# Kernel tuning notes

Hardware: AMD Instinct MI355X
Metric: run time of the kernel (lower is better)

Reference implementation:

```python
import jax, jax.numpy as jnp
import numpy as np

N, E, G = 100000, 300000, 2048
H, C = 4, 64            # heads, per-head channels; hidden = H*C = 256
NODE_DIM, EDGE_DIM, HID = 256, 64, 256
NEG_SLOPE = 0.2
L = 3


def setup_inputs() -> dict:
    key = jax.random.key(0)
    ks = jax.random.split(key, 24)
    s = 0.05
    x = jax.random.normal(ks[0], (N, NODE_DIM), jnp.float32)
    src = jax.random.randint(ks[1], (E,), 0, N)
    dst = jax.random.randint(ks[2], (E,), 0, N)
    dst = jnp.where(src == dst, (dst + 1) % N, dst)  # no pre-existing self loops
    edge_index = jnp.stack([src, dst]).astype(jnp.int32)
    edge_attr = jax.random.normal(ks[3], (E, EDGE_DIM), jnp.float32)
    batch = jnp.sort(jax.random.randint(ks[4], (N,), 0, G)).astype(jnp.int32)
    # GATv2 layer params stacked over L layers (in_dim == HID for all layers)
    Wl = jax.random.normal(ks[5], (L, NODE_DIM, HID), jnp.float32) * s
    bl = jax.random.normal(ks[6], (L, HID), jnp.float32) * s
    Wr = jax.random.normal(ks[7], (L, NODE_DIM, HID), jnp.float32) * s
    br = jax.random.normal(ks[8], (L, HID), jnp.float32) * s
    We = jax.random.normal(ks[9], (L, EDGE_DIM, HID), jnp.float32) * s
    att = jax.random.normal(ks[10], (L, H, C), jnp.float32) * s
    bias = jax.random.normal(ks[11], (L, HID), jnp.float32) * s
    # predictor MLP
    Wp1 = jax.random.normal(ks[12], (HID, HID // 2), jnp.float32) * s
    bp1 = jax.random.normal(ks[13], (HID // 2,), jnp.float32) * s
    Wp2 = jax.random.normal(ks[14], (HID // 2, 1), jnp.float32) * s
    bp2 = jax.random.normal(ks[15], (1,), jnp.float32) * s
    return {"x": x, "edge_index": edge_index, "edge_attr": edge_attr, "batch": batch,
            "Wl": Wl, "bl": bl, "Wr": Wr, "br": br, "We": We, "att": att, "bias": bias,
            "Wp1": Wp1, "bp1": bp1, "Wp2": Wp2, "bp2": bp2}


def _gatv2_layer(x, src, dst, eattr, Wl, bl, Wr, br, We, att, bias):
    n = x.shape[0]
    xl = (x @ Wl + bl).reshape(n, H, C)  # lin_l (source side)
    xr = (x @ Wr + br).reshape(n, H, C)  # lin_r (target side)
    e = (eattr @ We).reshape(-1, H, C)   # lin_edge (no bias)
    m = jax.nn.leaky_relu(xl[src] + xr[dst] + e, NEG_SLOPE)  # [Etot,H,C]
    logits = jnp.einsum('ehc,hc->eh', m, att)                # [Etot,H]
    # segment softmax over destination nodes
    lmax = jax.ops.segment_max(logits, dst, num_segments=n)
    p = jnp.exp(logits - lmax[dst])
    denom = jax.ops.segment_sum(p, dst, num_segments=n)
    alpha = p / (denom[dst] + 1e-16)
    out = jax.ops.segment_sum(xl[src] * alpha[:, :, None], dst, num_segments=n)
    return out.reshape(n, H * C) + bias


def reference(x, edge_index, edge_attr, batch, Wl, bl, Wr, br, We, att, bias, Wp1, bp1, Wp2, bp2):
    n = x.shape[0]
    src, dst = edge_index[0], edge_index[1]
    # add self loops with edge_attr fill_value='mean' (PyG default)
    loop = jnp.arange(n, dtype=src.dtype)
    src_f = jnp.concatenate([src, loop])
    dst_f = jnp.concatenate([dst, loop])
    eattr_f = jnp.concatenate([edge_attr, jnp.broadcast_to(edge_attr.mean(0), (n, edge_attr.shape[1]))], 0)
    for l in range(L):
        x = jax.nn.relu(_gatv2_layer(x, src_f, dst_f, eattr_f,
                                     Wl[l], bl[l], Wr[l], br[l], We[l], att[l], bias[l]))
    # global mean pool over graphs
    sums = jax.ops.segment_sum(x, batch, num_segments=G)
    cnt = jax.ops.segment_sum(jnp.ones((n,), x.dtype), batch, num_segments=G)
    pooled = sums / jnp.maximum(cnt, 1.0)[:, None]
    h = jax.nn.relu(pooled @ Wp1 + bp1)
    return (h @ Wp2 + bp2).squeeze(-1)  # [G]
```

## Files before the change

### kernel.cpp

```cpp
#include <hip/hip_runtime.h>
#include <hip/hip_bf16.h>

#define N_ 100000
#define E_ 300000
#define ETOT 400000
#define G_ 2048
#define NB_SCAN 98
#define NB_SCAN2 391

typedef __attribute__((ext_vector_type(8))) short bf16x8;
typedef __attribute__((ext_vector_type(4))) float f32x4;

__device__ __forceinline__ short f2bf(float f) {
    __hip_bfloat16 h = __float2bfloat16(f);
    return *reinterpret_cast<short*>(&h);
}
__device__ __forceinline__ float bf2f(short s) {
    __hip_bfloat16 h = *reinterpret_cast<__hip_bfloat16*>(&s);
    return __bfloat162float(h);
}

typedef __attribute__((address_space(1))) void* gas_ptr;
typedef __attribute__((address_space(3))) void* las_ptr;
__device__ __forceinline__ void gload16(const void* g, void* l) {
    __builtin_amdgcn_global_load_lds((gas_ptr)g, (las_ptr)l, 16, 0, 0);
}

__device__ __forceinline__ int xcd_swz(int bid, int nwg) {
    int q = nwg >> 3, rr = nwg & 7;
    int xcd = bid & 7, i = bid >> 3;
    return (xcd < rr) ? xcd * (q + 1) + i : rr * (q + 1) + (xcd - rr) * q + i;
}

__global__ __launch_bounds__(256) void mean_kernel(const float* __restrict__ ea, float* __restrict__ meansum) {
    __shared__ float s[256];
    int tid = threadIdx.x;
    int col = tid & 63, rg = tid >> 6;
    float acc = 0.f;
    for (long long row = (long long)blockIdx.x * 4 + rg; row < E_; row += (long long)gridDim.x * 4)
        acc += ea[row * 64 + col];
    s[tid] = acc;
    __syncthreads();
    if (tid < 64) atomicAdd(meansum + tid, s[tid] + s[tid + 64] + s[tid + 128] + s[tid + 192]);
}

__global__ __launch_bounds__(256) void loope_kernel(const float* __restrict__ meansum,
                                                    const float* __restrict__ We_l,
                                                    float* __restrict__ loope) {
    int c = threadIdx.x;
    float acc = 0.f;
    const float invE = 1.0f / (float)E_;
    for (int k = 0; k < 64; k++) acc += (meansum[k] * invE) * We_l[k * 256 + c];
    loope[c] = acc;
}

__device__ __forceinline__ int swz_col(int row, int k) {
    int c = (k >> 3) & 3;
    int s = (row >> 1) & 3;
    return (k & ~31) | ((c ^ s) << 3) | (k & 7);
}

__global__ __launch_bounds__(256) void prep_wcat_kernel(const float* __restrict__ Wl, const float* __restrict__ Wr,
                                                        short* __restrict__ hi, short* __restrict__ lo) {
    int idx = blockIdx.x * 256 + threadIdx.x;
    if (idx >= 3 * 512 * 256) return;
    int l = idx / (512 * 256);
    int rem = idx % (512 * 256);
    int n = rem >> 8, k = rem & 255;
    float v = (n < 256) ? Wl[((size_t)l * 256 + k) * 256 + n]
                        : Wr[((size_t)l * 256 + k) * 256 + (n - 256)];
    short h = f2bf(v);
    size_t o = (size_t)l * 512 * 256 + (size_t)n * 256 + swz_col(n, k);
    hi[o] = h;
    lo[o] = f2bf(v - bf2f(h));
}

__global__ __launch_bounds__(256) void prep_we_kernel(const float* __restrict__ We,
                                                      short* __restrict__ hi) {
    int idx = blockIdx.x * 256 + threadIdx.x;
    if (idx >= 3 * 256 * 64) return;
    int l = idx / (256 * 64);
    int rem = idx % (256 * 64);
    int n = rem >> 6, k = rem & 63;
    float v = We[((size_t)l * 64 + k) * 256 + n];
    hi[(size_t)l * 256 * 64 + (size_t)n * 64 + swz_col(n, k)] = f2bf(v);
}

__global__ __launch_bounds__(256) void split_x_kernel(const float* __restrict__ in,
                                                      short* __restrict__ hi, short* __restrict__ lo) {
    int idx = blockIdx.x * 256 + threadIdx.x;
    if (idx >= N_ * 32) return;
    int gm = idx >> 5, cw = idx & 31;
    int c = cw & 3, win = cw >> 2;
    int s = (gm >> 1) & 3;
    const float* src = in + (size_t)gm * 256 + (win << 5) + (c << 3);
    float4 f0 = *(const float4*)src;
    float4 f1 = *(const float4*)(src + 4);
    float f[8] = {f0.x, f0.y, f0.z, f0.w, f1.x, f1.y, f1.z, f1.w};
    bf16x8 vh, vl;
#pragma unroll
    for (int j = 0; j < 8; j++) {
        short h = f2bf(f[j]);
        vh[j] = h;
        vl[j] = f2bf(f[j] - bf2f(h));
    }
    size_t o = (size_t)gm * 256 + (win << 5) + ((c ^ s) << 3);
    *(bf16x8*)(hi + o) = vh;
    *(bf16x8*)(lo + o) = vl;
}

__global__ __launch_bounds__(256) void split_e_kernel(const float* __restrict__ in, short* __restrict__ hi,
                                                      const int* __restrict__ pose, const int* __restrict__ rnk) {
    int idx = blockIdx.x * 256 + threadIdx.x;
    if (idx >= E_ * 8) return;
    int e = idx >> 3, cw = idx & 7;
    int c = cw & 3, win = cw >> 2;
    int rk = rnk[pose[e]];
    int s = (rk >> 1) & 3;
    const float* src = in + (size_t)e * 64 + (win << 5) + (c << 3);
    float4 f0 = *(const float4*)src;
    float4 f1 = *(const float4*)(src + 4);
    float f[8] = {f0.x, f0.y, f0.z, f0.w, f1.x, f1.y, f1.z, f1.w};
    bf16x8 vh;
#pragma unroll
    for (int j = 0; j < 8; j++) vh[j] = f2bf(f[j]);
    *(bf16x8*)(hi + (size_t)rk * 64 + (win << 5) + ((c ^ s) << 3)) = vh;
}

__global__ __launch_bounds__(256) void hist_kernel(const int* __restrict__ ei, int* __restrict__ deg) {
    int e = blockIdx.x * 256 + threadIdx.x;
    if (e >= ETOT) return;
    int d = (e < E_) ? ei[E_ + e] : (e - E_);
    atomicAdd(deg + d, 1);
}

__global__ __launch_bounds__(256) void scanA_kernel(const int* __restrict__ deg, int* __restrict__ off,
                                                    int* __restrict__ bsum) {
    __shared__ int s[256];
    int tid = threadIdx.x;
    int base = blockIdx.x * 1024 + tid * 4;
    int v[4];
#pragma unroll
    for (int i = 0; i < 4; i++) v[i] = (base + i < N_) ? deg[base + i] : 0;
    v[1] += v[0]; v[2] += v[1]; v[3] += v[2];
    s[tid] = v[3];
    __syncthreads();
    for (int o = 1; o < 256; o <<= 1) {
        int t = (tid >= o) ? s[tid - o] : 0;
        __syncthreads();
        s[tid] += t;
        __syncthreads();
    }
    int prev = tid ? s[tid - 1] : 0;
#pragma unroll
    for (int i = 0; i < 4; i++)
        if (base + i < N_) off[base + i + 1] = prev + v[i];
    if (tid == 255) bsum[blockIdx.x] = s[255];
}

__global__ void scanB_kernel(int* __restrict__ bsum, int n) {
    if (threadIdx.x == 0) {
        int run = 0;
        for (int i = 0; i < n; i++) { int t = bsum[i]; bsum[i] = run; run += t; }
    }
}

__global__ __launch_bounds__(256) void scanC_kernel(int* __restrict__ off, const int* __restrict__ bsum) {
    int i = blockIdx.x * 256 + threadIdx.x;
    if (i < N_) {
        off[i + 1] += bsum[i >> 10];
        if (i == 0) off[0] = 0;
    }
}

__global__ __launch_bounds__(256) void scatter_kernel(const int* __restrict__ ei, int* __restrict__ cursor,
                                                      int* __restrict__ srcs, int* __restrict__ dstp,
                                                      int* __restrict__ pose) {
    int e = blockIdx.x * 256 + threadIdx.x;
    if (e >= ETOT) return;
    int s, d;
    if (e < E_) { s = ei[e]; d = ei[E_ + e]; }
    else        { s = e - E_; d = s; }
    int pos = atomicAdd(cursor + d, 1);
    srcs[pos] = s;
    dstp[pos] = d;
    pose[e] = pos;
}

__global__ __launch_bounds__(256) void scanA2_kernel(const int* __restrict__ srcs, const int* __restrict__ dstp,
                                                     int* __restrict__ rnk, int* __restrict__ bsum2) {
    __shared__ int sm[256];
    int tid = threadIdx.x;
    int base = blockIdx.x * 1024 + tid * 4;
    int v[4];
#pragma unroll
    for (int i = 0; i < 4; i++) {
        int p = base + i;
        v[i] = (p < ETOT && srcs[p] != dstp[p]) ? 1 : 0;
    }
    int incl1 = v[0] + v[1], incl2 = incl1 + v[2], incl3 = incl2 + v[3];
    sm[tid] = incl3;
    __syncthreads();
    for (int o = 1; o < 256; o <<= 1) {
        int t = (tid >= o) ? sm[tid - o] : 0;
        __syncthreads();
        sm[tid] += t;
        __syncthreads();
    }
    int prev = tid ? sm[tid - 1] : 0;
    int incl[4] = {v[0], incl1, incl2, incl3};
#pragma unroll
    for (int i = 0; i < 4; i++) {
        int p = base + i;
        if (p < ETOT) rnk[p] = prev + incl[i] - v[i];
    }
    if (tid == 255) bsum2[blockIdx.x] = sm[255];
}

__global__ __launch_bounds__(256) void scanC2_kernel(int* __restrict__ rnk, const int* __restrict__ bsum2) {
    int p = blockIdx.x * 256 + threadIdx.x;
    if (p < ETOT) rnk[p] += bsum2[p >> 10];
}

__global__ __launch_bounds__(256) void compact_kernel(const int* __restrict__ srcs, const int* __restrict__ dstp,
                                                      const int* __restrict__ rnk,
                                                      int* __restrict__ srcs_c, int* __restrict__ dstp_c,
                                                      int* __restrict__ posr_c) {
    int pos = blockIdx.x * 256 + threadIdx.x;
    if (pos >= ETOT) return;
    int s = srcs[pos], d = dstp[pos];
    if (s != d) {
        int rk = rnk[pos];
        srcs_c[rk] = s;
        dstp_c[rk] = d;
        posr_c[rk] = pos;
    }
}

#define BM 128

__global__ __launch_bounds__(256, 4) void mfma_gemm_node(
    const short* __restrict__ Ahi_g, const short* __restrict__ Alo_g,
    const short* __restrict__ Bhi_g, const short* __restrict__ Blo_g,
    float* __restrict__ C0, short* __restrict__ C0b, short* __restrict__ C1b,
    const float* __restrict__ bias0, const float* __restrict__ bias1,
    int M, int K) {
    __shared__ short Ah[BM * 32];
    __shared__ short Bh[BM * 32];
    __shared__ short Al[BM * 32];
    __shared__ short Bl[BM * 32];

    const int v = xcd_swz(blockIdx.x, gridDim.x);
    const int n0 = (v & 3) * BM;
    const int m0 = (v >> 2) * BM;
    const int tid = threadIdx.x;
    const int wave = tid >> 6, lane = tid & 63;
    const int wm = (wave >> 1) << 6, wn = (wave & 1) << 6;
    const int r = lane & 15, q = lane >> 4;
    const int qs = (q ^ ((r >> 1) & 3)) << 3;

    const int srow = (wave << 5) + (lane >> 2);
    const int sch = (lane & 3) << 3;
    int ga0 = m0 + srow;       if (ga0 > M - 1) ga0 = M - 1;
    int ga1 = m0 + srow + 16;  if (ga1 > M - 1) ga1 = M - 1;
    const int offA0 = ga0 * K + sch;
    const int offA1 = ga1 * K + sch;
    const int offB0 = (n0 + srow) * K + sch;
    const int offB1 = (n0 + srow + 16) * K + sch;
    short* lA0 = &Ah[(wave << 5) * 32];
    short* lA1 = lA0 + 16 * 32;
    short* lB0 = &Bh[(wave << 5) * 32];
    short* lB1 = lB0 + 16 * 32;
    short* lAl0 = &Al[(wave << 5) * 32];
    short* lAl1 = lAl0 + 16 * 32;
    short* lBl0 = &Bl[(wave << 5) * 32];
    short* lBl1 = lBl0 + 16 * 32;

    f32x4 acc[4][4];
#pragma unroll
    for (int i = 0; i < 4; i++)
#pragma unroll
        for (int j = 0; j < 4; j++) acc[i][j] = (f32x4){0.f, 0.f, 0.f, 0.f};

    for (int k0 = 0; k0 < K; k0 += 32) {
        gload16(Ahi_g + offA0 + k0, lA0);
        gload16(Ahi_g + offA1 + k0, lA1);
        gload16(Bhi_g + offB0 + k0, lB0);
        gload16(Bhi_g + offB1 + k0, lB1);
        gload16(Alo_g + offA0 + k0, lAl0);
        gload16(Alo_g + offA1 + k0, lAl1);
        gload16(Blo_g + offB0 + k0, lBl0);
        gload16(Blo_g + offB1 + k0, lBl1);
        __syncthreads();

        bf16x8 ah[4], bh[4];
#pragma unroll
        for (int f = 0; f < 4; f++) {
            ah[f] = *(const bf16x8*)(Ah + (wm + f * 16 + r) * 32 + qs);
            bh[f] = *(const bf16x8*)(Bh + (wn + f * 16 + r) * 32 + qs);
        }
#pragma unroll
        for (int fm = 0; fm < 4; fm++)
#pragma unroll
            for (int fn = 0; fn < 4; fn++)
                acc[fm][fn] = __builtin_amdgcn_mfma_f32_16x16x32_bf16(ah[fm], bh[fn], acc[fm][fn], 0, 0, 0);
        bf16x8 t[4];
#pragma unroll
        for (int f = 0; f < 4; f++) t[f] = *(const bf16x8*)(Bl + (wn + f * 16 + r) * 32 + qs);
#pragma unroll
        for (int fm = 0; fm < 4; fm++)
#pragma unroll
            for (int fn = 0; fn < 4; fn++)
                acc[fm][fn] = __builtin_amdgcn_mfma_f32_16x16x32_bf16(ah[fm], t[fn], acc[fm][fn], 0, 0, 0);
#pragma unroll
        for (int f = 0; f < 4; f++) t[f] = *(const bf16x8*)(Al + (wm + f * 16 + r) * 32 + qs);
#pragma unroll
        for (int fm = 0; fm < 4; fm++)
#pragma unroll
            for (int fn = 0; fn < 4; fn++)
                acc[fm][fn] = __builtin_amdgcn_mfma_f32_16x16x32_bf16(t[fm], bh[fn], acc[fm][fn], 0, 0, 0);
        __syncthreads();
    }

    const bool second = (n0 >= 256);
    const int ncol = second ? n0 - 256 : n0;
    const float* bs = second ? bias1 : bias0;
#pragma unroll
    for (int fm = 0; fm < 4; fm++) {
#pragma unroll
        for (int fn = 0; fn < 4; fn++) {
            int col = ncol + wn + fn * 16 + r;
            float bv = bs[col];
#pragma unroll
            for (int g = 0; g < 4; g++) {
                int row = m0 + wm + fm * 16 + q * 4 + g;
                if (row < M) {
                    float vv = acc[fm][fn][g] + bv;
                    size_t o = (size_t)row * 256 + col;
                    if (second) {
                        C1b[o] = f2bf(vv);
                    } else {
                        C0[o] = vv;
                        C0b[o] = f2bf(vv);
                    }
                }
            }
        }
    }
}

__global__ __launch_bounds__(256, 4) void edge_fused_kernel(
    const short* __restrict__ Ag,
    const short* __restrict__ Bg,
    const int* __restrict__ srcs_c, const int* __restrict__ dstp_c, const int* __restrict__ posr_c,
    const short* __restrict__ xlb, const short* __restrict__ xrb,
    const float* __restrict__ att,
    float* __restrict__ plog) {
    __shared__ short smem[128 * 132];
    short* Ah = smem;
    short* Bh = smem + 128 * 32;
    short* Ct = smem;

    const int v = xcd_swz(blockIdx.x, gridDim.x);
    const int n0 = (v & 1) << 7;
    const int m0 = (v >> 1) << 7;
    const int tid = threadIdx.x;
    const int wave = tid >> 6, lane = tid & 63;
    const int wm = (wave >> 1) << 6, wn = (wave & 1) << 6;
    const int r = lane & 15, q = lane >> 4;
    const int qs = (q ^ ((r >> 1) & 3)) << 3;

    const int srow = (wave << 5) + (lane >> 2);
    const int sch = (lane & 3) << 3;
    int ga0 = m0 + srow;       if (ga0 > E_ - 1) ga0 = E_ - 1;
    int ga1 = m0 + srow + 16;  if (ga1 > E_ - 1) ga1 = E_ - 1;
    const int offA0 = ga0 * 64 + sch;
    const int offA1 = ga1 * 64 + sch;
    const int offB0 = (n0 + srow) * 64 + sch;
    const int offB1 = (n0 + srow + 16) * 64 + sch;
    short* lA0 = Ah + (wave << 5) * 32;
    short* lA1 = lA0 + 16 * 32;
    short* lB0 = Bh + (wave << 5) * 32;
    short* lB1 = lB0 + 16 * 32;

    f32x4 acc[4][4];
#pragma unroll
    for (int i = 0; i < 4; i++)
#pragma unroll
        for (int j = 0; j < 4; j++) acc[i][j] = (f32x4){0.f, 0.f, 0.f, 0.f};

#pragma unroll
    for (int k0 = 0; k0 < 64; k0 += 32) {
        gload16(Ag + offA0 + k0, lA0);
        gload16(Ag + offA1 + k0, lA1);
        gload16(Bg + offB0 + k0, lB0);
        gload16(Bg + offB1 + k0, lB1);
        __syncthreads();
        bf16x8 ah[4], bh[4];
#pragma unroll
        for (int f = 0; f < 4; f++) {
            ah[f] = *(const bf16x8*)(Ah + (wm + f * 16 + r) * 32 + qs);
            bh[f] = *(const bf16x8*)(Bh + (wn + f * 16 + r) * 32 + qs);
        }
#pragma unroll
        for (int fm = 0; fm < 4; fm++)
#pragma unroll
            for (int fn = 0; fn < 4; fn++)
                acc[fm][fn] = __builtin_amdgcn_mfma_f32_16x16x32_bf16(ah[fm], bh[fn], acc[fm][fn], 0, 0, 0);
        __syncthreads();
    }

#pragma unroll
    for (int fm = 0; fm < 4; fm++)
#pragma unroll
        for (int fn = 0; fn < 4; fn++)
#pragma unroll
            for (int g = 0; g < 4; g++)
                Ct[(wm + fm * 16 + q * 4 + g) * 132 + wn + fn * 16 + r] = f2bf(acc[fm][fn][g]);
    __syncthreads();

    const int half = lane >> 5;
    const int hsel = (lane >> 4) & 1;
    const int sub = lane & 15;
    const int colL = (hsel << 6) + (sub << 2);
    const float4 w = *(const float4*)(att + n0 + colL);
    const int hglob = (n0 >> 6) + hsel;
    for (int it = 0; it < 16; it++) {
        int prow = (wave << 5) + (it << 1) + half;
        int ec = m0 + prow;
        bool valid = (ec < E_);
        int s = 0, d = 0, pos = 0;
        if (valid) { s = srcs_c[ec]; d = dstp_c[ec]; pos = posr_c[ec]; }
        short4 ev = *(const short4*)(Ct + prow * 132 + colL);
        short4 a = valid ? *(const short4*)(xlb + (size_t)s * 256 + n0 + colL) : make_short4(0, 0, 0, 0);
        short4 b = valid ? *(const short4*)(xrb + (size_t)d * 256 + n0 + colL) : make_short4(0, 0, 0, 0);
        float m0v = bf2f(a.x) + bf2f(b.x) + bf2f(ev.x);
        float m1v = bf2f(a.y) + bf2f(b.y) + bf2f(ev.y);
        float m2v = bf2f(a.z) + bf2f(b.z) + bf2f(ev.z);
        float m3v = bf2f(a.w) + bf2f(b.w) + bf2f(ev.w);
        m0v = (m0v > 0.f) ? m0v : 0.2f * m0v;
        m1v = (m1v > 0.f) ? m1v : 0.2f * m1v;
        m2v = (m2v > 0.f) ? m2v : 0.2f * m2v;
        m3v = (m3v > 0.f) ? m3v : 0.2f * m3v;
        float rr = m0v * w.x + m1v * w.y + m2v * w.z + m3v * w.w;
#pragma unroll
        for (int o = 1; o < 16; o <<= 1) rr += __shfl_xor(rr, o, 64);
        if (valid && sub == 0)
            plog[(size_t)pos * 4 + hglob] = rr;
    }
}

__global__ __launch_bounds__(256) void self_logits_kernel(const short* __restrict__ xlb, const short* __restrict__ xrb,
                                                          const float* __restrict__ loope, const float* __restrict__ att,
                                                          const int* __restrict__ pose,
                                                          float* __restrict__ plog) {
    int wid = threadIdx.x >> 6;
    int lane = threadIdx.x & 63;
    int n = blockIdx.x * 4 + wid;
    if (n >= N_) return;
    short4 a = *(const short4*)(xlb + (size_t)n * 256 + lane * 4);
    short4 b = *(const short4*)(xrb + (size_t)n * 256 + lane * 4);
    float4 c = *(const float4*)(loope + lane * 4);
    float4 w = *(const float4*)(att + lane * 4);
    float m0 = bf2f(a.x) + bf2f(b.x) + c.x;
    float m1 = bf2f(a.y) + bf2f(b.y) + c.y;
    float m2 = bf2f(a.z) + bf2f(b.z) + c.z;
    float m3 = bf2f(a.w) + bf2f(b.w) + c.w;
    m0 = (m0 > 0.f) ? m0 : 0.2f * m0;
    m1 = (m1 > 0.f) ? m1 : 0.2f * m1;
    m2 = (m2 > 0.f) ? m2 : 0.2f * m2;
    m3 = (m3 > 0.f) ? m3 : 0.2f * m3;
    float r = m0 * w.x + m1 * w.y + m2 * w.z + m3 * w.w;
#pragma unroll
    for (int o = 1; o < 16; o <<= 1) r += __shfl_xor(r, o, 64);
    int pos = pose[E_ + n];
    if ((lane & 15) == 0)
        plog[(size_t)pos * 4 + (lane >> 4)] = r;
}

__global__ __launch_bounds__(256) void softmax_node_kernel(const int* __restrict__ off,
                                                           const float* __restrict__ plog,
                                                           float* __restrict__ alpha) {
    int wid = threadIdx.x >> 6, lane = threadIdx.x & 63;
    int d = blockIdx.x * 4 + wid;
    if (d >= N_) return;
    int s0 = off[d], s1 = off[d + 1];
    int sub = lane & 15, h = lane >> 4;
    float mx = -3.4e38f;
    for (int i = s0 + sub; i < s1; i += 16)
        mx = fmaxf(mx, plog[(size_t)i * 4 + h]);
#pragma unroll
    for (int o = 1; o < 16; o <<= 1) mx = fmaxf(mx, __shfl_xor(mx, o, 64));
    float sum = 0.f;
    for (int i = s0 + sub; i < s1; i += 16)
        sum += expf(plog[(size_t)i * 4 + h] - mx);
#pragma unroll
    for (int o = 1; o < 16; o <<= 1) sum += __shfl_xor(sum, o, 64);
    float dn = sum + 1e-16f;
    for (int i = s0 + sub; i < s1; i += 16)
        alpha[(size_t)i * 4 + h] = expf(plog[(size_t)i * 4 + h] - mx) / dn;
}

__global__ __launch_bounds__(256) void agg_kernel(const float* __restrict__ xl, const float* __restrict__ alpha,
                                                  const int* __restrict__ off, const int* __restrict__ srcs,
                                                  const float* __restrict__ bias,
                                                  float* __restrict__ xf32, short* __restrict__ xhi,
                                                  short* __restrict__ xlo) {
    int wid = threadIdx.x >> 6, lane = threadIdx.x & 63;
    int d = blockIdx.x * 4 + wid;
    if (d >= N_) return;
    int s0 = off[d], s1 = off[d + 1];
    int col = lane << 2;
    int h = lane >> 4;
    float4 acc = make_float4(0.f, 0.f, 0.f, 0.f);
    int i = s0;
    for (; i + 2 <= s1; i += 2) {
        int a0 = srcs[i], a1 = srcs[i + 1];
        float w0 = alpha[(size_t)i * 4 + h];
        float w1 = alpha[(size_t)(i + 1) * 4 + h];
        float4 x0 = *(const float4*)(xl + (size_t)a0 * 256 + col);
        float4 x1 = *(const float4*)(xl + (size_t)a1 * 256 + col);
        acc.x += w0 * x0.x + w1 * x1.x;
        acc.y += w0 * x0.y + w1 * x1.y;
        acc.z += w0 * x0.z + w1 * x1.z;
        acc.w += w0 * x0.w + w1 * x1.w;
    }
    if (i < s1) {
        int a0 = srcs[i];
        float w0 = alpha[(size_t)i * 4 + h];
        float4 x0 = *(const float4*)(xl + (size_t)a0 * 256 + col);
        acc.x += w0 * x0.x;
        acc.y += w0 * x0.y;
        acc.z += w0 * x0.z;
        acc.w += w0 * x0.w;
    }
    float4 bv = *(const float4*)(bias + col);
    float4 v;
    v.x = acc.x + bv.x; v.x = v.x > 0.f ? v.x : 0.f;
    v.y = acc.y + bv.y; v.y = v.y > 0.f ? v.y : 0.f;
    v.z = acc.z + bv.z; v.z = v.z > 0.f ? v.z : 0.f;
    v.w = acc.w + bv.w; v.w = v.w > 0.f ? v.w : 0.f;
    if (xf32) *(float4*)(xf32 + (size_t)d * 256 + col) = v;
    if (xhi) {
        int c = (lane >> 1) & 3, s = (d >> 1) & 3;
        size_t o = (size_t)d * 256 + (col & ~31) + ((c ^ s) << 3) + (col & 7);
        float f[4] = {v.x, v.y, v.z, v.w};
        short4 hh, ll;
        short* ph = (short*)&hh;
        short* pl = (short*)&ll;
#pragma unroll
        for (int j = 0; j < 4; j++) {
            ph[j] = f2bf(f[j]);
            pl[j] = f2bf(f[j] - bf2f(ph[j]));
        }
        *(short4*)(xhi + o) = hh;
        *(short4*)(xlo + o) = ll;
    }
}

__device__ __forceinline__ int lbound(const int* __restrict__ a, int n, int v) {
    int lo = 0, hi = n;
    while (lo < hi) { int mid = (lo + hi) >> 1; if (a[mid] < v) lo = mid + 1; else hi = mid; }
    return lo;
}

__global__ __launch_bounds__(256) void pool_mlp_kernel(const float* __restrict__ x, const int* __restrict__ batch,
                                                       const float* __restrict__ Wp1, const float* __restrict__ bp1,
                                                       const float* __restrict__ Wp2, const float* __restrict__ bp2,
                                                       float* __restrict__ out) {
    int g = blockIdx.x;
    int t = threadIdx.x;
    int lo = lbound(batch, N_, g);
    int hi = lbound(batch, N_, g + 1);
    float sum = 0.f;
    for (int n = lo; n < hi; n++) sum += x[(size_t)n * 256 + t];
    int cnt = hi - lo;
    float pooled = sum / (float)(cnt > 1 ? cnt : 1);
    __shared__ float sp[256];
    __shared__ float sh[128];
    __shared__ float sw[4];
    sp[t] = pooled;
    __syncthreads();
    if (t < 128) {
        float a = bp1[t];
        for (int k = 0; k < 256; k++) a += sp[k] * Wp1[k * 128 + t];
        sh[t] = a > 0.f ? a : 0.f;
    }
    __syncthreads();
    float v = (t < 128) ? sh[t] * Wp2[t] : 0.f;
#pragma unroll
    for (int o = 32; o; o >>= 1) v += __shfl_xor(v, o, 64);
    if ((t & 63) == 0) sw[t >> 6] = v;
    __syncthreads();
    if (t == 0) out[g] = sw[0] + sw[1] + sw[2] + sw[3] + bp2[0];
}

#define XHI_OFF  ((size_t)0)
#define XLO_OFF  (XHI_OFF + (size_t)N_ * 256 * 2)
#define W0_OFF   ((size_t)0)
#define XL_OFF   (XLO_OFF + (size_t)N_ * 256 * 2)
#define XLB_OFF  (XL_OFF + (size_t)N_ * 256 * 4)
#define XRB_OFF  (XLB_OFF + (size_t)N_ * 256 * 2)
#define LG_OFF   (XRB_OFF + (size_t)N_ * 256 * 2)
#define AL_OFF   (LG_OFF + (size_t)ETOT * 4 * 4)
#define LM_OFF   (AL_OFF + (size_t)ETOT * 4 * 4)
#define DN_OFF   (LM_OFF + (size_t)N_ * 4 * 4)
#define DG_OFF   (DN_OFF + (size_t)N_ * 4 * 4)
#define OF_OFF   (DG_OFF + (size_t)N_ * 4)
#define CU_OFF   (OF_OFF + (size_t)(N_ + 32) * 4)
#define SR_OFF   (CU_OFF + (size_t)N_ * 4)
#define DP_OFF   (SR_OFF + (size_t)ETOT * 4)
#define PE_OFF   (DP_OFF + (size_t)ETOT * 4)
#define RN_OFF   (PE_OFF + (size_t)ETOT * 4)
#define SC_OFF   (RN_OFF + (size_t)ETOT * 4)
#define DC_OFF   (SC_OFF + (size_t)E_ * 4)
#define PC_OFF   (DC_OFF + (size_t)E_ * 4)
#define BS_OFF   (PC_OFF + (size_t)E_ * 4)
#define BS2_OFF  (BS_OFF + (size_t)512)
#define MS_OFF   (BS2_OFF + (size_t)2048)
#define LE_OFF   (MS_OFF + (size_t)256)
#define WCH_OFF  (LE_OFF + (size_t)2048)
#define WCL_OFF  (WCH_OFF + (size_t)3 * 512 * 256 * 2)
#define WEH_OFF  (WCL_OFF + (size_t)3 * 512 * 256 * 2)
#define EAT_OFF  (WEH_OFF + (size_t)3 * 256 * 64 * 2)

extern "C" void kernel_launch(void* const* d_in, const int* in_sizes, int n_in,
                              void* d_out, int out_size, void* d_ws, size_t ws_size,
                              hipStream_t stream) {
    const float* x     = (const float*)d_in[0];
    const int*   ei    = (const int*)d_in[1];
    const float* eattr = (const float*)d_in[2];
    const int*   batch = (const int*)d_in[3];
    const float* Wl    = (const float*)d_in[4];
    const float* bl    = (const float*)d_in[5];
    const float* Wr    = (const float*)d_in[6];
    const float* br    = (const float*)d_in[7];
    const float* We    = (const float*)d_in[8];
    const float* att   = (const float*)d_in[9];
    const float* bias  = (const float*)d_in[10];
    const float* Wp1   = (const float*)d_in[11];
    const float* bp1   = (const float*)d_in[12];
    const float* Wp2   = (const float*)d_in[13];
    const float* bp2   = (const float*)d_in[14];

    char* ws = (char*)d_ws;
    short*    xhi     = (short*)(ws + XHI_OFF);
    short*    xlo     = (short*)(ws + XLO_OFF);
    float*    w0      = (float*)(ws + W0_OFF);
    float*    xl      = (float*)(ws + XL_OFF);
    short*    xlb     = (short*)(ws + XLB_OFF);
    short*    xrb     = (short*)(ws + XRB_OFF);
    float*    plog    = (float*)(ws + LG_OFF);
    float*    alpha   = (float*)(ws + AL_OFF);
    int*      deg     = (int*)(ws + DG_OFF);
    int*      off     = (int*)(ws + OF_OFF);
    int*      cursor  = (int*)(ws + CU_OFF);
    int*      srcs    = (int*)(ws + SR_OFF);
    int*      dstp    = (int*)(ws + DP_OFF);
    int*      pose    = (int*)(ws + PE_OFF);
    int*      rnk     = (int*)(ws + RN_OFF);
    int*      srcs_c  = (int*)(ws + SC_OFF);
    int*      dstp_c  = (int*)(ws + DC_OFF);
    int*      posr_c  = (int*)(ws + PC_OFF);
    int*      bsum    = (int*)(ws + BS_OFF);
    int*      bsum2   = (int*)(ws + BS2_OFF);
    float*    meansum = (float*)(ws + MS_OFF);
    float*    loope   = (float*)(ws + LE_OFF);
    short*    wcatH   = (short*)(ws + WCH_OFF);
    short*    wcatL   = (short*)(ws + WCL_OFF);
    short*    weH     = (short*)(ws + WEH_OFF);
    short*    eattrb  = (short*)(ws + EAT_OFF);

    hipMemsetAsync(meansum, 0, 64 * 4, stream);
    hipMemsetAsync(deg, 0, (size_t)N_ * 4, stream);
    mean_kernel<<<512, 256, 0, stream>>>(eattr, meansum);
    prep_wcat_kernel<<<(3 * 512 * 256 + 255) / 256, 256, 0, stream>>>(Wl, Wr, wcatH, wcatL);
    prep_we_kernel<<<(3 * 256 * 64 + 255) / 256, 256, 0, stream>>>(We, weH);
    split_x_kernel<<<(N_ * 32 + 255) / 256, 256, 0, stream>>>(x, xhi, xlo);
    hist_kernel<<<(ETOT + 255) / 256, 256, 0, stream>>>(ei, deg);
    scanA_kernel<<<NB_SCAN, 256, 0, stream>>>(deg, off, bsum);
    scanB_kernel<<<1, 64, 0, stream>>>(bsum, NB_SCAN);
    scanC_kernel<<<(N_ + 255) / 256, 256, 0, stream>>>(off, bsum);
    hipMemcpyAsync(cursor, off, (size_t)N_ * 4, hipMemcpyDeviceToDevice, stream);
    scatter_kernel<<<(ETOT + 255) / 256, 256, 0, stream>>>(ei, cursor, srcs, dstp, pose);
    scanA2_kernel<<<NB_SCAN2, 256, 0, stream>>>(srcs, dstp, rnk, bsum2);
    scanB_kernel<<<1, 64, 0, stream>>>(bsum2, NB_SCAN2);
    scanC2_kernel<<<(ETOT + 255) / 256, 256, 0, stream>>>(rnk, bsum2);
    compact_kernel<<<(ETOT + 255) / 256, 256, 0, stream>>>(srcs, dstp, rnk, srcs_c, dstp_c, posr_c);
    split_e_kernel<<<(E_ * 8 + 255) / 256, 256, 0, stream>>>(eattr, eattrb, pose, rnk);

    const int mtN = (N_ + BM - 1) / BM;
    const int nwgN = 4 * mtN;
    const int mtE = (E_ + 127) / 128;
    const int nwgE = 2 * mtE;

    for (int l = 0; l < 3; l++) {
        const float* We_l = We + (size_t)l * 64 * 256;
        const float* att_l = att + (size_t)l * 256;
        loope_kernel<<<1, 256, 0, stream>>>(meansum, We_l, loope);
        mfma_gemm_node<<<nwgN, 256, 0, stream>>>(
            xhi, xlo, wcatH + (size_t)l * 512 * 256, wcatL + (size_t)l * 512 * 256,
            xl, xlb, xrb, bl + (size_t)l * 256, br + (size_t)l * 256, N_, 256);
        edge_fused_kernel<<<nwgE, 256, 0, stream>>>(
            eattrb, weH + (size_t)l * 256 * 64, srcs_c, dstp_c, posr_c, xlb, xrb, att_l, plog);
        self_logits_kernel<<<(N_ + 3) / 4, 256, 0, stream>>>(xlb, xrb, loope, att_l, pose, plog);
        softmax_node_kernel<<<(N_ + 3) / 4, 256, 0, stream>>>(off, plog, alpha);
        agg_kernel<<<(N_ + 3) / 4, 256, 0, stream>>>(
            xl, alpha, off, srcs, bias + (size_t)l * 256,
            (l == 2) ? w0 : nullptr,
            (l < 2) ? xhi : nullptr,
            (l < 2) ? xlo : nullptr);
    }

    pool_mlp_kernel<<<G_, 256, 0, stream>>>(w0, batch, Wp1, bp1, Wp2, bp2, (float*)d_out);
}
```

Before: 1.630 ms.

## Fuse softmax into aggregation and store xl as interleaved bf16 hi/lo pairs

The node GEMM now writes xl as an interleaved bf16 hi/lo split (8 shorts per 4 columns) instead of separate fp32 and bf16 copies. The edge-logit and self-logit kernels read the hi half from this buffer. The softmax kernel is merged into the aggregation kernel, which recomputes the normalized weights from the logits on the fly, so the alpha array and one launch per layer go away. This removes one full write and read of alpha and one fp32 xl store. The cost is strided hi-only reads in the logit kernels and a little extra exp work in aggregation.

```diff
diff --git a/kernel.cpp b/kernel.cpp
--- a/kernel.cpp
+++ b/kernel.cpp
@@ -242,7 +242,7 @@
 __global__ __launch_bounds__(256, 4) void mfma_gemm_node(
     const short* __restrict__ Ahi_g, const short* __restrict__ Alo_g,
     const short* __restrict__ Bhi_g, const short* __restrict__ Blo_g,
-    float* __restrict__ C0, short* __restrict__ C0b, short* __restrict__ C1b,
+    short* __restrict__ Csp, short* __restrict__ C1b,
     const float* __restrict__ bias0, const float* __restrict__ bias1,
     int M, int K) {
     __shared__ short Ah[BM * 32];
@@ -336,12 +336,14 @@
                 int row = m0 + wm + fm * 16 + q * 4 + g;
                 if (row < M) {
                     float vv = acc[fm][fn][g] + bv;
-                    size_t o = (size_t)row * 256 + col;
                     if (second) {
-                        C1b[o] = f2bf(vv);
+                        C1b[(size_t)row * 256 + col] = f2bf(vv);
                     } else {
-                        C0[o] = vv;
-                        C0b[o] = f2bf(vv);
+                        short hh = f2bf(vv);
+                        short ll = f2bf(vv - bf2f(hh));
+                        size_t o2 = (size_t)row * 512 + ((size_t)(col >> 2) << 3) + (col & 3);
+                        Csp[o2] = hh;
+                        Csp[o2 + 4] = ll;
                     }
                 }
             }
@@ -353,7 +355,7 @@
     const short* __restrict__ Ag,
     const short* __restrict__ Bg,
     const int* __restrict__ srcs_c, const int* __restrict__ dstp_c, const int* __restrict__ posr_c,
-    const short* __restrict__ xlb, const short* __restrict__ xrb,
+    const short* __restrict__ xsp, const short* __restrict__ xrb,
     const float* __restrict__ att,
     float* __restrict__ plog) {
     __shared__ short smem[128 * 132];
@@ -425,6 +427,7 @@
     const int colL = (hsel << 6) + (sub << 2);
     const float4 w = *(const float4*)(att + n0 + colL);
     const int hglob = (n0 >> 6) + hsel;
+    const int gc2 = (n0 + colL) << 1;
     for (int it = 0; it < 16; it++) {
         int prow = (wave << 5) + (it << 1) + half;
         int ec = m0 + prow;
@@ -432,7 +435,7 @@
         int s = 0, d = 0, pos = 0;
         if (valid) { s = srcs_c[ec]; d = dstp_c[ec]; pos = posr_c[ec]; }
         short4 ev = *(const short4*)(Ct + prow * 132 + colL);
-        short4 a = valid ? *(const short4*)(xlb + (size_t)s * 256 + n0 + colL) : make_short4(0, 0, 0, 0);
+        short4 a = valid ? *(const short4*)(xsp + (size_t)s * 512 + gc2) : make_short4(0, 0, 0, 0);
         short4 b = valid ? *(const short4*)(xrb + (size_t)d * 256 + n0 + colL) : make_short4(0, 0, 0, 0);
         float m0v = bf2f(a.x) + bf2f(b.x) + bf2f(ev.x);
         float m1v = bf2f(a.y) + bf2f(b.y) + bf2f(ev.y);
@@ -450,7 +453,7 @@
     }
 }
 
-__global__ __launch_bounds__(256) void self_logits_kernel(const short* __restrict__ xlb, const short* __restrict__ xrb,
+__global__ __launch_bounds__(256) void self_logits_kernel(const short* __restrict__ xsp, const short* __restrict__ xrb,
                                                           const float* __restrict__ loope, const float* __restrict__ att,
                                                           const int* __restrict__ pose,
                                                           float* __restrict__ plog) {
@@ -458,7 +461,7 @@
     int lane = threadIdx.x & 63;
     int n = blockIdx.x * 4 + wid;
     if (n >= N_) return;
-    short4 a = *(const short4*)(xlb + (size_t)n * 256 + lane * 4);
+    short4 a = *(const short4*)(xsp + (size_t)n * 512 + (lane << 3));
     short4 b = *(const short4*)(xrb + (size_t)n * 256 + lane * 4);
     float4 c = *(const float4*)(loope + lane * 4);
     float4 w = *(const float4*)(att + lane * 4);
@@ -478,9 +481,11 @@
         plog[(size_t)pos * 4 + (lane >> 4)] = r;
 }
 
-__global__ __launch_bounds__(256) void softmax_node_kernel(const int* __restrict__ off,
-                                                           const float* __restrict__ plog,
-                                                           float* __restrict__ alpha) {
+__global__ __launch_bounds__(256) void agg_kernel(const short* __restrict__ xsp, const float* __restrict__ plog,
+                                                  const int* __restrict__ off, const int* __restrict__ srcs,
+                                                  const float* __restrict__ bias,
+                                                  float* __restrict__ xf32, short* __restrict__ xhi,
+                                                  short* __restrict__ xlo) {
     int wid = threadIdx.x >> 6, lane = threadIdx.x & 63;
     int d = blockIdx.x * 4 + wid;
     if (d >= N_) return;
@@ -497,43 +502,38 @@
 #pragma unroll
     for (int o = 1; o < 16; o <<= 1) sum += __shfl_xor(sum, o, 64);
     float dn = sum + 1e-16f;
-    for (int i = s0 + sub; i < s1; i += 16)
-        alpha[(size_t)i * 4 + h] = expf(plog[(size_t)i * 4 + h] - mx) / dn;
-}
-
-__global__ __launch_bounds__(256) void agg_kernel(const float* __restrict__ xl, const float* __restrict__ alpha,
-                                                  const int* __restrict__ off, const int* __restrict__ srcs,
-                                                  const float* __restrict__ bias,
-                                                  float* __restrict__ xf32, short* __restrict__ xhi,
-                                                  short* __restrict__ xlo) {
-    int wid = threadIdx.x >> 6, lane = threadIdx.x & 63;
-    int d = blockIdx.x * 4 + wid;
-    if (d >= N_) return;
-    int s0 = off[d], s1 = off[d + 1];
-    int col = lane << 2;
-    int h = lane >> 4;
+
     float4 acc = make_float4(0.f, 0.f, 0.f, 0.f);
     int i = s0;
     for (; i + 2 <= s1; i += 2) {
         int a0 = srcs[i], a1 = srcs[i + 1];
-        float w0 = alpha[(size_t)i * 4 + h];
-        float w1 = alpha[(size_t)(i + 1) * 4 + h];
-        float4 x0 = *(const float4*)(xl + (size_t)a0 * 256 + col);
-        float4 x1 = *(const float4*)(xl + (size_t)a1 * 256 + col);
-        acc.x += w0 * x0.x + w1 * x1.x;
-        acc.y += w0 * x0.y + w1 * x1.y;
-        acc.z += w0 * x0.z + w1 * x1.z;
-        acc.w += w0 * x0.w + w1 * x1.w;
+        float w0 = expf(plog[(size_t)i * 4 + h] - mx) / dn;
+        float w1 = expf(plog[(size_t)(i + 1) * 4 + h] - mx) / dn;
+        bf16x8 v0 = *(const bf16x8*)(xsp + (size_t)a0 * 512 + (lane << 3));
+        bf16x8 v1 = *(const bf16x8*)(xsp + (size_t)a1 * 512 + (lane << 3));
+        float x00 = bf2f(v0[0]) + bf2f(v0[4]);
+        float x01 = bf2f(v0[1]) + bf2f(v0[5]);
+        float x02 = bf2f(v0[2]) + bf2f(v0[6]);
+        float x03 = bf2f(v0[3]) + bf2f(v0[7]);
+        float x10 = bf2f(v1[0]) + bf2f(v1[4]);
+        float x11 = bf2f(v1[1]) + bf2f(v1[5]);
+        float x12 = bf2f(v1[2]) + bf2f(v1[6]);
+        float x13 = bf2f(v1[3]) + bf2f(v1[7]);
+        acc.x += w0 * x00 + w1 * x10;
+        acc.y += w0 * x01 + w1 * x11;
+        acc.z += w0 * x02 + w1 * x12;
+        acc.w += w0 * x03 + w1 * x13;
     }
     if (i < s1) {
         int a0 = srcs[i];
-        float w0 = alpha[(size_t)i * 4 + h];
-        float4 x0 = *(const float4*)(xl + (size_t)a0 * 256 + col);
-        acc.x += w0 * x0.x;
-        acc.y += w0 * x0.y;
-        acc.z += w0 * x0.z;
-        acc.w += w0 * x0.w;
-    }
+        float w0 = expf(plog[(size_t)i * 4 + h] - mx) / dn;
+        bf16x8 v0 = *(const bf16x8*)(xsp + (size_t)a0 * 512 + (lane << 3));
+        acc.x += w0 * (bf2f(v0[0]) + bf2f(v0[4]));
+        acc.y += w0 * (bf2f(v0[1]) + bf2f(v0[5]));
+        acc.z += w0 * (bf2f(v0[2]) + bf2f(v0[6]));
+        acc.w += w0 * (bf2f(v0[3]) + bf2f(v0[7]));
+    }
+    int col = lane << 2;
     float4 bv = *(const float4*)(bias + col);
     float4 v;
     v.x = acc.x + bv.x; v.x = v.x > 0.f ? v.x : 0.f;
@@ -598,14 +598,10 @@
 #define XHI_OFF  ((size_t)0)
 #define XLO_OFF  (XHI_OFF + (size_t)N_ * 256 * 2)
 #define W0_OFF   ((size_t)0)
-#define XL_OFF   (XLO_OFF + (size_t)N_ * 256 * 2)
-#define XLB_OFF  (XL_OFF + (size_t)N_ * 256 * 4)
-#define XRB_OFF  (XLB_OFF + (size_t)N_ * 256 * 2)
+#define XSP_OFF  (XLO_OFF + (size_t)N_ * 256 * 2)
+#define XRB_OFF  (XSP_OFF + (size_t)N_ * 512 * 2)
 #define LG_OFF   (XRB_OFF + (size_t)N_ * 256 * 2)
-#define AL_OFF   (LG_OFF + (size_t)ETOT * 4 * 4)
-#define LM_OFF   (AL_OFF + (size_t)ETOT * 4 * 4)
-#define DN_OFF   (LM_OFF + (size_t)N_ * 4 * 4)
-#define DG_OFF   (DN_OFF + (size_t)N_ * 4 * 4)
+#define DG_OFF   (LG_OFF + (size_t)ETOT * 4 * 4)
 #define OF_OFF   (DG_OFF + (size_t)N_ * 4)
 #define CU_OFF   (OF_OFF + (size_t)(N_ + 32) * 4)
 #define SR_OFF   (CU_OFF + (size_t)N_ * 4)
@@ -647,11 +643,9 @@
     short*    xhi     = (short*)(ws + XHI_OFF);
     short*    xlo     = (short*)(ws + XLO_OFF);
     float*    w0      = (float*)(ws + W0_OFF);
-    float*    xl      = (float*)(ws + XL_OFF);
-    short*    xlb     = (short*)(ws + XLB_OFF);
+    short*    xsp     = (short*)(ws + XSP_OFF);
     short*    xrb     = (short*)(ws + XRB_OFF);
     float*    plog    = (float*)(ws + LG_OFF);
-    float*    alpha   = (float*)(ws + AL_OFF);
     int*      deg     = (int*)(ws + DG_OFF);
     int*      off     = (int*)(ws + OF_OFF);
     int*      cursor  = (int*)(ws + CU_OFF);
@@ -700,13 +694,12 @@
         loope_kernel<<<1, 256, 0, stream>>>(meansum, We_l, loope);
         mfma_gemm_node<<<nwgN, 256, 0, stream>>>(
             xhi, xlo, wcatH + (size_t)l * 512 * 256, wcatL + (size_t)l * 512 * 256,
-            xl, xlb, xrb, bl + (size_t)l * 256, br + (size_t)l * 256, N_, 256);
+            xsp, xrb, bl + (size_t)l * 256, br + (size_t)l * 256, N_, 256);
         edge_fused_kernel<<<nwgE, 256, 0, stream>>>(
-            eattrb, weH + (size_t)l * 256 * 64, srcs_c, dstp_c, posr_c, xlb, xrb, att_l, plog);
-        self_logits_kernel<<<(N_ + 3) / 4, 256, 0, stream>>>(xlb, xrb, loope, att_l, pose, plog);
-        softmax_node_kernel<<<(N_ + 3) / 4, 256, 0, stream>>>(off, plog, alpha);
+            eattrb, weH + (size_t)l * 256 * 64, srcs_c, dstp_c, posr_c, xsp, xrb, att_l, plog);
+        self_logits_kernel<<<(N_ + 3) / 4, 256, 0, stream>>>(xsp, xrb, loope, att_l, pose, plog);
         agg_kernel<<<(N_ + 3) / 4, 256, 0, stream>>>(
-            xl, alpha, off, srcs, bias + (size_t)l * 256,
+            xsp, plog, off, srcs, bias + (size_t)l * 256,
             (l == 2) ? w0 : nullptr,
             (l < 2) ? xhi : nullptr,
             (l < 2) ? xlo : nullptr);
```

Result: faster. 1.463 ms (-10.2%).
